# Kernel optimization log

Hardware: AMD Instinct MI355X
Metric: run time of the kernel (lower is better)

The kernel has to match this reference:

```python
import jax, jax.numpy as jnp
import numpy as np

B, T, C = 2, 2048, 2048
N_HEAD, N_KV = 32, 8
HD = C // N_HEAD  # 64
N_REP = N_HEAD // N_KV  # 4
ROPE_BASE = 10000.0


def setup_inputs() -> dict:
    key = jax.random.key(0)
    ks = jax.random.split(key, 5)
    s = 0.02
    return {
        "x": jax.random.normal(ks[0], (B, T, C), jnp.float32),
        "Wq": jax.random.normal(ks[1], (C, N_HEAD * HD), jnp.float32) * s,
        "Wk": jax.random.normal(ks[2], (C, N_KV * HD), jnp.float32) * s,
        "Wv": jax.random.normal(ks[3], (C, N_KV * HD), jnp.float32) * s,
        "Wo": jax.random.normal(ks[4], (N_HEAD * HD, C), jnp.float32) * s,
    }


def _rope_cos_sin(seq_len, head_dim, dtype):
    inv_freq = 1.0 / (ROPE_BASE ** (jnp.arange(0, head_dim, 2, dtype=jnp.float32) / head_dim))
    t = jnp.arange(seq_len, dtype=jnp.float32)
    freqs = t[:, None] * inv_freq[None, :]           # (T, hd/2)
    emb = jnp.concatenate([freqs, freqs], axis=-1)    # (T, hd)
    return jnp.cos(emb).astype(dtype), jnp.sin(emb).astype(dtype)


def _rotate_half(x):
    h = x.shape[-1] // 2
    return jnp.concatenate([-x[..., h:], x[..., :h]], axis=-1)


def reference(x, Wq, Wk, Wv, Wo):
    b, t, c = x.shape
    # projections -> (B, H, T, hd)
    q = (x @ Wq).reshape(b, t, N_HEAD, HD).transpose(0, 2, 1, 3)
    k = (x @ Wk).reshape(b, t, N_KV, HD).transpose(0, 2, 1, 3)
    v = (x @ Wv).reshape(b, t, N_KV, HD).transpose(0, 2, 1, 3)

    cos, sin = _rope_cos_sin(t, HD, x.dtype)          # (T, hd)
    q = q * cos + _rotate_half(q) * sin
    k = k * cos + _rotate_half(k) * sin

    # GQA: group query heads (B, n_kv, n_rep, T, hd) against shared KV (no repeat materialization)
    qg = q.reshape(b, N_KV, N_REP, t, HD)
    scale = 1.0 / jnp.sqrt(jnp.asarray(HD, x.dtype))
    scores = jnp.einsum('bgrqd,bgkd->bgrqk', qg, k) * scale  # (B, n_kv, n_rep, T, T)
    causal = jnp.tril(jnp.ones((t, t), bool))
    scores = jnp.where(causal, scores, jnp.asarray(-jnp.inf, scores.dtype))
    probs = jax.nn.softmax(scores, axis=-1)
    out = jnp.einsum('bgrqk,bgkd->bgrqd', probs, v)          # (B, n_kv, n_rep, T, hd)
    out = out.reshape(b, N_HEAD, t, HD).transpose(0, 2, 1, 3).reshape(b, t, N_HEAD * HD)
    return out @ Wo
```

## Files before the change

kernel.cpp:

```cpp
#include <hip/hip_runtime.h>
#include <stdint.h>

#define Bn 2
#define Tn 2048
#define Cn 2048
#define NHEAD 32
#define NKVH 8
#define HDIM 64
#define Mn (Bn*Tn)
#define NQKV 3072
#define KOFF 2048
#define VOFF 2560

typedef __attribute__((ext_vector_type(8))) short bf16x8;
typedef __attribute__((ext_vector_type(4))) float f32x4;

#define AS1 __attribute__((address_space(1)))
#define AS3 __attribute__((address_space(3)))
#define GLOAD_LDS16(g, l) __builtin_amdgcn_global_load_lds((const AS1 void*)(g), (AS3 void*)(l), 16, 0, 0)

#define SCL 0.18033688f

__device__ __forceinline__ unsigned short f2bf(float f) {
    union { float f; unsigned u; } v; v.f = f;
    return (unsigned short)((v.u + 0x7fffu + ((v.u >> 16) & 1u)) >> 16);
}
__device__ __forceinline__ float bf2f(unsigned short b) {
    union { unsigned u; float f; } v; v.u = ((unsigned)b) << 16;
    return v.f;
}

__global__ void convert_f32_bf16(const float* __restrict__ src,
                                 unsigned short* __restrict__ dst, int n4) {
    int i = blockIdx.x * blockDim.x + threadIdx.x;
    if (i >= n4) return;
    float4 f = ((const float4*)src)[i];
    ushort4 o;
    o.x = f2bf(f.x); o.y = f2bf(f.y); o.z = f2bf(f.z); o.w = f2bf(f.w);
    ((ushort4*)dst)[i] = o;
}

__global__ void transpose_convert(const float* __restrict__ src,
                                  unsigned short* __restrict__ dst, int K, int N) {
    __shared__ float tile[32][33];
    int k0 = blockIdx.x * 32, n0 = blockIdx.y * 32;
    int tx = threadIdx.x, ty = threadIdx.y;
    #pragma unroll
    for (int yy = 0; yy < 32; yy += 8)
        tile[ty + yy][tx] = src[(size_t)(k0 + ty + yy) * N + n0 + tx];
    __syncthreads();
    #pragma unroll
    for (int yy = 0; yy < 32; yy += 8)
        dst[(size_t)(n0 + ty + yy) * K + k0 + tx] = f2bf(tile[tx][ty + yy]);
}

__global__ void rope_tables(float* __restrict__ ct, float* __restrict__ st) {
    int i = blockIdx.x * blockDim.x + threadIdx.x;
    int t = i >> 5, d = i & 31;
    float invf = powf(10000.0f, -(float)d / 32.0f);
    float f = (float)t * invf;
    ct[i] = cosf(f);
    st[i] = sinf(f);
}

__global__ void rope_apply(unsigned short* __restrict__ qkv,
                           const float* __restrict__ ct, const float* __restrict__ st) {
    int i = blockIdx.x * blockDim.x + threadIdx.x;
    int p = i & 31;
    int h = (i >> 5) % 40;
    int bt = i / (40 * 32);
    int t = bt & (Tn - 1);
    size_t base = (size_t)bt * NQKV + h * 64;
    float v0 = bf2f(qkv[base + p]);
    float v1 = bf2f(qkv[base + p + 32]);
    float c = ct[t * 32 + p], s = st[t * 32 + p];
    float scl = (h < 32) ? SCL : 1.0f;
    qkv[base + p]      = f2bf((v0 * c - v1 * s) * scl);
    qkv[base + p + 32] = f2bf((v1 * c + v0 * s) * scl);
}

__global__ void transpose_v(const unsigned short* __restrict__ qkv,
                            unsigned short* __restrict__ vt) {
    __shared__ unsigned short tile[32][33];
    int t0 = blockIdx.x * 32;
    int b = blockIdx.y >> 3, kvh = blockIdx.y & 7;
    int d0 = blockIdx.z * 32;
    int tx = threadIdx.x, ty = threadIdx.y;
    #pragma unroll
    for (int yy = 0; yy < 32; yy += 8)
        tile[ty + yy][tx] = qkv[(size_t)(b * Tn + t0 + ty + yy) * NQKV + VOFF + kvh * 64 + d0 + tx];
    __syncthreads();
    #pragma unroll
    for (int yy = 0; yy < 32; yy += 8)
        vt[(size_t)((b * 8 + kvh) * 64 + d0 + ty + yy) * Tn + t0 + tx] = tile[tx][ty + yy];
}

template <bool BF16OUT>
__global__ __launch_bounds__(256) void gemm_bt(
    const unsigned short* __restrict__ A, const unsigned short* __restrict__ Bt,
    unsigned short* __restrict__ outb, float* __restrict__ outf, int M, int N, int K) {
    __shared__ unsigned short sA[128 * 32];
    __shared__ unsigned short sB[128 * 32];
    int tid = threadIdx.x;
    int wid = tid >> 6, lane = tid & 63;
    int wr = wid >> 1, wc = wid & 1;
    int g = lane >> 4, r16 = lane & 15;
    int brow = blockIdx.y * 128, bcol = blockIdx.x * 128;

    f32x4 acc[4][4];
    #pragma unroll
    for (int m = 0; m < 4; m++)
        #pragma unroll
        for (int n = 0; n < 4; n++) acc[m][n] = (f32x4){0.f, 0.f, 0.f, 0.f};

    for (int k0 = 0; k0 < K; k0 += 32) {
        __syncthreads();
        #pragma unroll
        for (int j = 0; j < 2; j++) {
            int cs = wid * 2 + j;
            int bo = cs * 1024 + lane * 16;
            int row = bo >> 6;
            int ce = (bo & 63) >> 1;
            const unsigned short* ga = A + (size_t)(brow + row) * K + k0 + ce;
            const unsigned short* gb = Bt + (size_t)(bcol + row) * K + k0 + ce;
            GLOAD_LDS16(ga, (char*)sA + cs * 1024);
            GLOAD_LDS16(gb, (char*)sB + cs * 1024);
        }
        __syncthreads();
        bf16x8 av[4], bv[4];
        #pragma unroll
        for (int m = 0; m < 4; m++)
            av[m] = *(const bf16x8*)&sA[(wr * 64 + m * 16 + r16) * 32 + g * 8];
        #pragma unroll
        for (int n = 0; n < 4; n++)
            bv[n] = *(const bf16x8*)&sB[(wc * 64 + n * 16 + r16) * 32 + g * 8];
        #pragma unroll
        for (int m = 0; m < 4; m++)
            #pragma unroll
            for (int n = 0; n < 4; n++)
                acc[m][n] = __builtin_amdgcn_mfma_f32_16x16x32_bf16(av[m], bv[n], acc[m][n], 0, 0, 0);
    }

    #pragma unroll
    for (int m = 0; m < 4; m++) {
        #pragma unroll
        for (int n = 0; n < 4; n++) {
            int row0 = brow + wr * 64 + m * 16 + g * 4;
            int col = bcol + wc * 64 + n * 16 + r16;
            #pragma unroll
            for (int r = 0; r < 4; r++) {
                float v = acc[m][n][r];
                if (BF16OUT)
                    outb[(size_t)(row0 + r) * N + col] = f2bf(v);
                else
                    outf[(size_t)(row0 + r) * N + col] = v;
            }
        }
    }
}

__device__ __forceinline__ void flash_step(
    const bf16x8 (&qf)[2], float (&pl)[4], f32x4 (&oo)[4],
    const unsigned short* __restrict__ sK, const unsigned short* __restrict__ sVt,
    unsigned short* __restrict__ sPw, int g, int r16, int wid, bool masked) {
    f32x4 s[4];
    #pragma unroll
    for (int n = 0; n < 4; n++) {
        s[n] = (f32x4){0.f, 0.f, 0.f, 0.f};
        #pragma unroll
        for (int kc = 0; kc < 2; kc++) {
            int kv = n * 16 + r16;
            int bo = (kv * 128 + kc * 64 + g * 16) ^ ((kv & 7) << 4);
            bf16x8 kf = *(const bf16x8*)((const char*)sK + bo);
            s[n] = __builtin_amdgcn_mfma_f32_16x16x32_bf16(qf[kc], kf, s[n], 0, 0, 0);
        }
    }
    if (masked) {
        #pragma unroll
        for (int n = 0; n < 4; n++)
            #pragma unroll
            for (int r = 0; r < 4; r++)
                s[n][r] = (n * 16 + r16 <= wid * 16 + g * 4 + r) ? s[n][r] : -1e30f;
    }
    #pragma unroll
    for (int n = 0; n < 4; n++)
        #pragma unroll
        for (int r = 0; r < 4; r++) s[n][r] = exp2f(s[n][r]);
    #pragma unroll
    for (int r = 0; r < 4; r++)
        pl[r] += (s[0][r] + s[1][r]) + (s[2][r] + s[3][r]);
    #pragma unroll
    for (int n = 0; n < 4; n++)
        #pragma unroll
        for (int r = 0; r < 4; r++) {
            int prow = g * 4 + r;
            int bo = (prow * 128 + (n * 16 + r16) * 2) ^ ((prow & 7) << 4);
            union { float f; unsigned u; } pv; pv.f = s[n][r];
            *(unsigned short*)((char*)sPw + bo) = (unsigned short)(pv.u >> 16);
        }
    #pragma unroll
    for (int dt = 0; dt < 4; dt++) {
        #pragma unroll
        for (int kc = 0; kc < 2; kc++) {
            int bo = (r16 * 128 + kc * 64 + g * 16) ^ ((r16 & 7) << 4);
            bf16x8 pf = *(const bf16x8*)((const char*)sPw + bo);
            int dd = dt * 16 + r16;
            int bo2 = (dd * 128 + kc * 64 + g * 16) ^ ((dd & 7) << 4);
            bf16x8 vf = *(const bf16x8*)((const char*)sVt + bo2);
            oo[dt] = __builtin_amdgcn_mfma_f32_16x16x32_bf16(pf, vf, oo[dt], 0, 0, 0);
        }
    }
}

__global__ __launch_bounds__(256, 4) void attn_fwd(
    const unsigned short* __restrict__ qkv, const unsigned short* __restrict__ vt,
    unsigned short* __restrict__ att) {
    __shared__ unsigned short sK[64 * 64];
    __shared__ unsigned short sVt[64 * 64];
    __shared__ unsigned short sP[4][16 * 64];

    int tid = threadIdx.x;
    int wid = tid >> 6, lane = tid & 63;
    int g = lane >> 4, r16 = lane & 15;
    int qp = blockIdx.x;
    int bh = blockIdx.y;
    int b = bh >> 5, qh = bh & 31, kvh = qh >> 2;
    int qtA = qp, qtB = 31 - qp;

    const unsigned short* base = qkv + (size_t)b * Tn * NQKV;
    const unsigned short* kg = base + KOFF + kvh * 64;
    const unsigned short* vg = vt + (size_t)((b * 8 + kvh) * 64) * Tn;

    bf16x8 qfA[2], qfB[2];
    {
        int qrA = qtA * 64 + wid * 16 + r16;
        int qrB = qtB * 64 + wid * 16 + r16;
        #pragma unroll
        for (int kc = 0; kc < 2; kc++) {
            qfA[kc] = *(const bf16x8*)(base + (size_t)qrA * NQKV + qh * 64 + kc * 32 + g * 8);
            qfB[kc] = *(const bf16x8*)(base + (size_t)qrB * NQKV + qh * 64 + kc * 32 + g * 8);
        }
    }

    float plA[4], plB[4];
    f32x4 oA[4], oB[4];
    #pragma unroll
    for (int r = 0; r < 4; r++) { plA[r] = 0.f; plB[r] = 0.f; }
    #pragma unroll
    for (int d = 0; d < 4; d++) {
        oA[d] = (f32x4){0.f, 0.f, 0.f, 0.f};
        oB[d] = (f32x4){0.f, 0.f, 0.f, 0.f};
    }

    unsigned short* sPw = &sP[wid][0];

    for (int j = 0; j <= qtB; j++) {
        __syncthreads();
        #pragma unroll
        for (int jj = 0; jj < 2; jj++) {
            int cs = wid * 2 + jj;
            int bo = cs * 1024 + lane * 16;
            int kvr = bo >> 7;
            int coff = (bo & 127) ^ ((kvr & 7) << 4);
            const unsigned short* gk = kg + (size_t)(j * 64 + kvr) * NQKV + (coff >> 1);
            GLOAD_LDS16(gk, (char*)sK + cs * 1024);
        }
        #pragma unroll
        for (int jj = 0; jj < 2; jj++) {
            int cs = wid * 2 + jj;
            int bo = cs * 1024 + lane * 16;
            int d = bo >> 7;
            int coff = (bo & 127) ^ ((d & 7) << 4);
            const unsigned short* gv = vg + (size_t)d * Tn + j * 64 + (coff >> 1);
            GLOAD_LDS16(gv, (char*)sVt + cs * 1024);
        }
        __syncthreads();

        if (j <= qtA) flash_step(qfA, plA, oA, sK, sVt, sPw, g, r16, wid, j == qtA);
        flash_step(qfB, plB, oB, sK, sVt, sPw, g, r16, wid, j == qtB);
    }

    float lA[4], lB[4];
    #pragma unroll
    for (int r = 0; r < 4; r++) {
        float vA = plA[r], vB = plB[r];
        #pragma unroll
        for (int msk = 1; msk < 16; msk <<= 1) {
            vA += __shfl_xor(vA, msk, 64);
            vB += __shfl_xor(vB, msk, 64);
        }
        lA[r] = 1.0f / vA;
        lB[r] = 1.0f / vB;
    }
    #pragma unroll
    for (int dt = 0; dt < 4; dt++)
        #pragma unroll
        for (int r = 0; r < 4; r++) {
            int qgA = qtA * 64 + wid * 16 + g * 4 + r;
            int qgB = qtB * 64 + wid * 16 + g * 4 + r;
            att[(size_t)(b * Tn + qgA) * Cn + qh * 64 + dt * 16 + r16] = f2bf(oA[dt][r] * lA[r]);
            att[(size_t)(b * Tn + qgB) * Cn + qh * 64 + dt * 16 + r16] = f2bf(oB[dt][r] * lB[r]);
        }
}

extern "C" void kernel_launch(void* const* d_in, const int* in_sizes, int n_in,
                              void* d_out, int out_size, void* d_ws, size_t ws_size,
                              hipStream_t stream) {
    const float* x  = (const float*)d_in[0];
    const float* Wq = (const float*)d_in[1];
    const float* Wk = (const float*)d_in[2];
    const float* Wv = (const float*)d_in[3];
    const float* Wo = (const float*)d_in[4];
    float* out = (float*)d_out;

    char* w = (char*)d_ws;
    unsigned short* Xb    = (unsigned short*)w; w += (size_t)Mn * Cn * 2;
    unsigned short* Wqkvt = (unsigned short*)w; w += (size_t)NQKV * Cn * 2;
    unsigned short* Wot   = (unsigned short*)w; w += (size_t)Cn * Cn * 2;
    unsigned short* QKV   = (unsigned short*)w; w += (size_t)Mn * NQKV * 2;
    unsigned short* ATT   = (unsigned short*)w; w += (size_t)Mn * Cn * 2;
    unsigned short* Vt    = (unsigned short*)w; w += (size_t)Bn * NKVH * HDIM * Tn * 2;
    float* ct = (float*)w; w += (size_t)Tn * 32 * 4;
    float* st = (float*)w; w += (size_t)Tn * 32 * 4;

    convert_f32_bf16<<<(Mn * Cn / 4) / 256, 256, 0, stream>>>(x, Xb, Mn * Cn / 4);
    dim3 tb(32, 8);
    transpose_convert<<<dim3(64, 64), tb, 0, stream>>>(Wq, Wqkvt, Cn, 2048);
    transpose_convert<<<dim3(64, 16), tb, 0, stream>>>(Wk, Wqkvt + (size_t)2048 * Cn, Cn, 512);
    transpose_convert<<<dim3(64, 16), tb, 0, stream>>>(Wv, Wqkvt + (size_t)2560 * Cn, Cn, 512);
    transpose_convert<<<dim3(64, 64), tb, 0, stream>>>(Wo, Wot, Cn, 2048);
    rope_tables<<<(Tn * 32) / 256, 256, 0, stream>>>(ct, st);

    gemm_bt<true><<<dim3(NQKV / 128, Mn / 128), 256, 0, stream>>>(Xb, Wqkvt, QKV, nullptr, Mn, NQKV, Cn);
    rope_apply<<<(Mn * 40 * 32) / 256, 256, 0, stream>>>(QKV, ct, st);
    transpose_v<<<dim3(Tn / 32, Bn * NKVH, 2), tb, 0, stream>>>(QKV, Vt);
    attn_fwd<<<dim3(16, Bn * NHEAD), 256, 0, stream>>>(QKV, Vt, ATT);
    gemm_bt<false><<<dim3(Cn / 128, Mn / 128), 256, 0, stream>>>(ATT, Wot, nullptr, out, Mn, Cn, Cn);
}
```

Baseline: 245.9 us.

## Double-buffer K/V tiles in attention loop to overlap loads with compute

Splits the shared-memory K and V^T tiles into two buffers. The first tile is preloaded before the loop, and each iteration issues async global-to-LDS loads for the next tile before running the flash steps on the current one. This drops one barrier per iteration and is meant to hide global memory latency behind MFMA work. It doubles K/V LDS use to about 40KB per block, which could limit occupancy at 4 blocks per CU. It also relies on the end-of-iteration barrier waiting for the outstanding async loads.

```diff
diff --git a/kernel.cpp b/kernel.cpp
--- a/kernel.cpp
+++ b/kernel.cpp
@@ -215,8 +215,8 @@
 __global__ __launch_bounds__(256, 4) void attn_fwd(
     const unsigned short* __restrict__ qkv, const unsigned short* __restrict__ vt,
     unsigned short* __restrict__ att) {
-    __shared__ unsigned short sK[64 * 64];
-    __shared__ unsigned short sVt[64 * 64];
+    __shared__ unsigned short sK[2][64 * 64];
+    __shared__ unsigned short sVt[2][64 * 64];
     __shared__ unsigned short sP[4][16 * 64];
 
     int tid = threadIdx.x;
@@ -231,6 +231,10 @@
     const unsigned short* kg = base + KOFF + kvh * 64;
     const unsigned short* vg = vt + (size_t)((b * 8 + kvh) * 64) * Tn;
 
+    int cs = 0, stg_coff = 0, stg_row = 0;
+    {
+    }
+
     bf16x8 qfA[2], qfB[2];
     {
         int qrA = qtA * 64 + wid * 16 + r16;
@@ -254,30 +258,39 @@
 
     unsigned short* sPw = &sP[wid][0];
 
+    #pragma unroll
+    for (int jj = 0; jj < 2; jj++) {
+        int c = wid * 2 + jj;
+        int bo = c * 1024 + lane * 16;
+        int row = bo >> 7;
+        int coff = (bo & 127) ^ ((row & 7) << 4);
+        GLOAD_LDS16(kg + (size_t)row * NQKV + (coff >> 1), (char*)&sK[0][0] + c * 1024);
+        GLOAD_LDS16(vg + (size_t)row * Tn + (coff >> 1), (char*)&sVt[0][0] + c * 1024);
+    }
+    __syncthreads();
+
+    int cur = 0;
     for (int j = 0; j <= qtB; j++) {
+        if (j < qtB) {
+            int nxt = cur ^ 1;
+            #pragma unroll
+            for (int jj = 0; jj < 2; jj++) {
+                int c = wid * 2 + jj;
+                int bo = c * 1024 + lane * 16;
+                int row = bo >> 7;
+                int coff = (bo & 127) ^ ((row & 7) << 4);
+                GLOAD_LDS16(kg + (size_t)((j + 1) * 64 + row) * NQKV + (coff >> 1),
+                            (char*)&sK[nxt][0] + c * 1024);
+                GLOAD_LDS16(vg + (size_t)row * Tn + (j + 1) * 64 + (coff >> 1),
+                            (char*)&sVt[nxt][0] + c * 1024);
+            }
+        }
+        const unsigned short* sKc = &sK[cur][0];
+        const unsigned short* sVc = &sVt[cur][0];
+        if (j <= qtA) flash_step(qfA, plA, oA, sKc, sVc, sPw, g, r16, wid, j == qtA);
+        flash_step(qfB, plB, oB, sKc, sVc, sPw, g, r16, wid, j == qtB);
         __syncthreads();
-        #pragma unroll
-        for (int jj = 0; jj < 2; jj++) {
-            int cs = wid * 2 + jj;
-            int bo = cs * 1024 + lane * 16;
-            int kvr = bo >> 7;
-            int coff = (bo & 127) ^ ((kvr & 7) << 4);
-            const unsigned short* gk = kg + (size_t)(j * 64 + kvr) * NQKV + (coff >> 1);
-            GLOAD_LDS16(gk, (char*)sK + cs * 1024);
-        }
-        #pragma unroll
-        for (int jj = 0; jj < 2; jj++) {
-            int cs = wid * 2 + jj;
-            int bo = cs * 1024 + lane * 16;
-            int d = bo >> 7;
-            int coff = (bo & 127) ^ ((d & 7) << 4);
-            const unsigned short* gv = vg + (size_t)d * Tn + j * 64 + (coff >> 1);
-            GLOAD_LDS16(gv, (char*)sVt + cs * 1024);
-        }
-        __syncthreads();
-
-        if (j <= qtA) flash_step(qfA, plA, oA, sK, sVt, sPw, g, r16, wid, j == qtA);
-        flash_step(qfB, plB, oB, sK, sVt, sPw, g, r16, wid, j == qtB);
+        cur ^= 1;
     }
 
     float lA[4], lB[4];
```

Result: no change. 246.8 us (+0.4%).
